# Optimization experiments

Measured on AMD Instinct MI355X. Metric: run time of the kernel, lower is better.

## Reference

```python
import jax, jax.numpy as jnp
import numpy as np

NUM_AUDIOS = 64
NODES_PER = 800
N = NUM_AUDIOS * NODES_PER  # 51200
DEG = 8
E = N * DEG  # 409600
IN_C, HID, OUT, HEADS = 512, 256, 256, 2
NEG_SLOPE = 0.2  # PyG GATConv default


def setup_inputs() -> dict:
    key = jax.random.key(0)
    ks = jax.random.split(key, 12)
    x = jax.random.normal(ks[0], (N, IN_C), jnp.float32)
    # edges strictly inside each audio's node block (PyG batching: no cross-graph edges)
    src_l = jax.random.randint(ks[1], (NUM_AUDIOS, NODES_PER * DEG), 0, NODES_PER)
    dst_l = jax.random.randint(ks[2], (NUM_AUDIOS, NODES_PER * DEG), 0, NODES_PER)
    off = (jnp.arange(NUM_AUDIOS) * NODES_PER)[:, None]
    edge_index = jnp.stack([(src_l + off).reshape(-1), (dst_l + off).reshape(-1)]).astype(jnp.int32)
    batch = jnp.repeat(jnp.arange(NUM_AUDIOS), NODES_PER).astype(jnp.int32)

    def gl(k, shape, fan):
        return (jax.random.normal(k, shape, jnp.float32) / np.sqrt(fan)).astype(jnp.float32)

    W1 = gl(ks[3], (IN_C, HEADS * HID), IN_C)
    a_s1 = gl(ks[4], (HEADS, HID), HID)
    a_d1 = gl(ks[5], (HEADS, HID), HID)
    b1 = jnp.zeros((HID,), jnp.float32)
    W2 = gl(ks[6], (HID, HEADS * OUT), HID)
    a_s2 = gl(ks[7], (HEADS, OUT), OUT)
    a_d2 = gl(ks[8], (HEADS, OUT), OUT)
    b2 = jnp.zeros((OUT,), jnp.float32)
    w_att = gl(ks[9], (OUT, 1), OUT)
    b_att = jnp.zeros((1,), jnp.float32)
    w_cls = gl(ks[10], (OUT, 2), OUT)
    b_cls = jnp.zeros((2,), jnp.float32)
    return dict(x=x, edge_index=edge_index, batch=batch,
                W1=W1, a_s1=a_s1, a_d1=a_d1, b1=b1,
                W2=W2, a_s2=a_s2, a_d2=a_d2, b2=b2,
                w_att=w_att, b_att=b_att, w_cls=w_cls, b_cls=b_cls)


def _gat(x, src, dst, W, a_s, a_d, b):
    """PyG GATConv(heads=H, concat=False): linear -> per-edge LeakyReLU scores ->
    softmax over incoming edges (with self-loops) -> scatter-sum -> head-mean + bias."""
    n = x.shape[0]
    H, C = a_s.shape
    h = (x @ W).reshape(n, H, C)                      # [N,H,C]
    al_s = jnp.einsum('nhc,hc->nh', h, a_s)           # [N,H]
    al_d = jnp.einsum('nhc,hc->nh', h, a_d)
    loop = jnp.arange(n, dtype=src.dtype)             # add self-loops (default)
    s = jnp.concatenate([src, loop])
    d = jnp.concatenate([dst, loop])
    e = jax.nn.leaky_relu(al_s[s] + al_d[d], NEG_SLOPE)  # [E+N,H]
    mx = jax.ops.segment_max(e, d, num_segments=n)
    w = jnp.exp(e - mx[d])
    den = jax.ops.segment_sum(w, d, num_segments=n)
    alpha = w / den[d]
    out = jax.ops.segment_sum(h[s] * alpha[:, :, None], d, num_segments=n)  # [N,H,C]
    return out.mean(axis=1) + b


def reference(x, edge_index, batch, W1, a_s1, a_d1, b1, W2, a_s2, a_d2, b2,
              w_att, b_att, w_cls, b_cls):
    src, dst = edge_index[0], edge_index[1]
    h = jax.nn.relu(_gat(x, src, dst, W1, a_s1, a_d1, b1))
    node_emb = _gat(h, src, dst, W2, a_s2, a_d2, b2)
    # per-audio temporal attention: softmax over nodes within each audio segment.
    # (edges never cross audio boundaries, so the per-subgraph GAT re-run in the
    #  original Python loop equals the full-graph GAT restricted to each segment.)
    logits = node_emb @ w_att + b_att                 # [N,1]
    mx = jax.ops.segment_max(logits, batch, num_segments=NUM_AUDIOS)
    w = jnp.exp(logits - mx[batch])
    den = jax.ops.segment_sum(w, batch, num_segments=NUM_AUDIOS)
    attn = w / den[batch]                             # [N,1]
    attended = jax.ops.segment_sum(attn * node_emb, batch, num_segments=NUM_AUDIOS)  # [A,OUT]
    audio_result = attended @ w_cls + b_cls           # [A,2]
    return node_emb, audio_result
```

## Files before the change

### kernel.cpp

```cpp
#include <hip/hip_runtime.h>
#include <cstdint>
#include <cstddef>

#define NUM_AUDIOS 64
#define NODES_PER  800
#define NN         51200
#define EE         409600

typedef __attribute__((ext_vector_type(8))) unsigned short ushort8;
typedef __attribute__((ext_vector_type(4))) unsigned short ushort4v;
typedef __attribute__((ext_vector_type(8))) __bf16 bf16x8;
typedef __attribute__((ext_vector_type(4))) float f32x4;

__device__ __forceinline__ float b2f(unsigned short h) {
  return __uint_as_float(((unsigned)h) << 16);
}
__device__ __forceinline__ unsigned short f2b(float f) {
  unsigned u = __float_as_uint(f);
  u += 0x7fffu + ((u >> 16) & 1u);
  return (unsigned short)(u >> 16);
}
__device__ __forceinline__ float lrelu(float v) { return v > 0.f ? v : 0.2f * v; }

#define P_AS1 0
#define P_AD1 512
#define P_B1  1024
#define P_AS2 1536
#define P_AD2 2048
#define P_B2  2560
#define P_WATT 3072
#define P_BATT 3328
#define P_WCLS 3336
#define P_BCLS 3848

__global__ __launch_bounds__(256) void detect_k(const unsigned short* __restrict__ x,
                                                int* __restrict__ flag) {
  __shared__ int s;
  if (threadIdx.x == 0) s = 0;
  __syncthreads();
  int big = 0;
  for (int i = threadIdx.x; i < 4096; i += 256) {
    const float v = b2f(x[i]);
    if (!(__builtin_fabsf(v) <= 1e4f)) big = 1;
  }
  if (big) atomicOr(&s, 1);
  __syncthreads();
  if (threadIdx.x == 0) *flag = s;
}

__global__ __launch_bounds__(256) void conv_x_k(const void* __restrict__ xraw,
                                                unsigned short* __restrict__ x16,
                                                const int* __restrict__ flag) {
  const size_t i = ((size_t)blockIdx.x * 256 + threadIdx.x) * 4;
  if (*flag) {
    const float4 v = *(const float4*)((const float*)xraw + i);
    ushort4v o;
    o[0] = f2b(v.x); o[1] = f2b(v.y); o[2] = f2b(v.z); o[3] = f2b(v.w);
    *(ushort4v*)(x16 + i) = o;
  } else {
    *(ushort4v*)(x16 + i) = *(const ushort4v*)((const unsigned short*)xraw + i);
  }
}

__global__ __launch_bounds__(256) void conv_params_k(
    const void* p0, const void* p1, const void* p2, const void* p3, const void* p4,
    const void* p5, const void* p6, const void* p7, const void* p8, const void* p9,
    unsigned short* __restrict__ dst, const int* __restrict__ flag) {
  const void* srcs[10] = {p0, p1, p2, p3, p4, p5, p6, p7, p8, p9};
  const int offs[10] = {P_AS1, P_AD1, P_B1, P_AS2, P_AD2, P_B2, P_WATT, P_BATT, P_WCLS, P_BCLS};
  const int lens[10] = {512, 512, 256, 512, 512, 256, 256, 1, 512, 2};
  const int b = blockIdx.x;
  const int f = *flag;
  for (int i = threadIdx.x; i < lens[b]; i += 256) {
    dst[offs[b] + i] = f ? f2b(((const float*)srcs[b])[i])
                         : ((const unsigned short*)srcs[b])[i];
  }
}

__global__ __launch_bounds__(256) void transpose_k(const void* __restrict__ W,
                                                   unsigned short* __restrict__ WT,
                                                   const int* __restrict__ flag,
                                                   int K, int Nc) {
  const int idx = blockIdx.x * 256 + threadIdx.x;
  const int n = idx / K, k = idx - n * K;
  WT[idx] = (*flag) ? f2b(((const float*)W)[(size_t)k * Nc + n])
                    : ((const unsigned short*)W)[(size_t)k * Nc + n];
}

__global__ __launch_bounds__(256) void gemm_bt(const unsigned short* __restrict__ A,
                                               const unsigned short* __restrict__ BT,
                                               unsigned short* __restrict__ C,
                                               int K, int Nn) {
  __shared__ unsigned short As[128 * 32];
  __shared__ unsigned short Bs[128 * 32];
  const int tid = threadIdx.x;
  const int wave = tid >> 6, lane = tid & 63;
  const int m0 = blockIdx.y * 128, n0 = blockIdx.x * 128;
  const int wm = wave >> 1, wn = wave & 1;
  const int row = lane & 15, quad = lane >> 4;
  f32x4 acc[4][4];
#pragma unroll
  for (int i = 0; i < 4; ++i)
#pragma unroll
    for (int j = 0; j < 4; ++j) acc[i][j] = (f32x4){0.f, 0.f, 0.f, 0.f};

  for (int k0 = 0; k0 < K; k0 += 32) {
#pragma unroll
    for (int r = 0; r < 2; ++r) {
      const int cc = r * 256 + wave * 64 + lane;
      const int arow = cc >> 2, kc = (cc & 3) * 8;
      __builtin_amdgcn_global_load_lds(
          (const __attribute__((address_space(1))) void*)(A + (size_t)(m0 + arow) * K + k0 + kc),
          (__attribute__((address_space(3))) void*)(As + (size_t)(r * 256 + wave * 64) * 8),
          16, 0, 0);
      __builtin_amdgcn_global_load_lds(
          (const __attribute__((address_space(1))) void*)(BT + (size_t)(n0 + arow) * K + k0 + kc),
          (__attribute__((address_space(3))) void*)(Bs + (size_t)(r * 256 + wave * 64) * 8),
          16, 0, 0);
    }
    __syncthreads();

    bf16x8 af[4], bq[4];
#pragma unroll
    for (int i = 0; i < 4; ++i) {
      af[i] = *(const bf16x8*)&As[(wm * 64 + i * 16 + row) * 32 + quad * 8];
      bq[i] = *(const bf16x8*)&Bs[(wn * 64 + i * 16 + row) * 32 + quad * 8];
    }
#pragma unroll
    for (int i = 0; i < 4; ++i)
#pragma unroll
      for (int j = 0; j < 4; ++j)
        acc[i][j] = __builtin_amdgcn_mfma_f32_16x16x32_bf16(af[i], bq[j], acc[i][j], 0, 0, 0);
    __syncthreads();
  }

  const int col = lane & 15;
#pragma unroll
  for (int i = 0; i < 4; ++i)
#pragma unroll
    for (int j = 0; j < 4; ++j)
#pragma unroll
      for (int r = 0; r < 4; ++r) {
        const int gm = m0 + wm * 64 + i * 16 + quad * 4 + r;
        const int gn = n0 + wn * 64 + j * 16 + col;
        C[(size_t)gm * Nn + gn] = f2b(acc[i][j][r]);
      }
}

__global__ __launch_bounds__(256) void al_k(const unsigned short* __restrict__ h,
                                            const unsigned short* __restrict__ a_s,
                                            const unsigned short* __restrict__ a_d,
                                            float* __restrict__ al_s, float* __restrict__ al_d) {
  const int wave = threadIdx.x >> 6, lane = threadIdx.x & 63;
  const int n = blockIdx.x * 4 + wave;
  const ushort8 hv = *(const ushort8*)&h[(size_t)n * 512 + lane * 8];
  const ushort8 sv = *(const ushort8*)&a_s[lane * 8];
  const ushort8 dv = *(const ushort8*)&a_d[lane * 8];
  float ps = 0.f, pd = 0.f;
#pragma unroll
  for (int j = 0; j < 8; ++j) {
    const float hf = b2f(hv[j]);
    ps += hf * b2f(sv[j]);
    pd += hf * b2f(dv[j]);
  }
#pragma unroll
  for (int off = 1; off < 32; off <<= 1) {
    ps += __shfl_xor(ps, off);
    pd += __shfl_xor(pd, off);
  }
  if ((lane & 31) == 0) {
    const int head = lane >> 5;
    al_s[n * 2 + head] = ps;
    al_d[n * 2 + head] = pd;
  }
}

__global__ __launch_bounds__(256) void hist_k(const int* __restrict__ dst, int* __restrict__ counts) {
  const int e = blockIdx.x * 256 + threadIdx.x;
  atomicAdd(&counts[dst[e]], 1);
}

__global__ __launch_bounds__(256) void rowptr_k(const int* __restrict__ counts, int* __restrict__ row_ptr) {
  __shared__ int sh[800];
  __shared__ int pre[200];
  const int a = blockIdx.x, t = threadIdx.x;
  for (int i = t; i < 800; i += 256) sh[i] = counts[a * 800 + i];
  __syncthreads();
  if (t < 200) pre[t] = sh[t * 4] + sh[t * 4 + 1] + sh[t * 4 + 2] + sh[t * 4 + 3];
  __syncthreads();
  if (t == 0) {
    int run = 0;
    for (int i = 0; i < 200; ++i) { const int v = pre[i]; pre[i] = run; run += v; }
  }
  __syncthreads();
  if (t < 200) {
    int b = a * 6400 + pre[t];
#pragma unroll
    for (int j = 0; j < 4; ++j) { row_ptr[a * 800 + t * 4 + j] = b; b += sh[t * 4 + j]; }
  }
}

__global__ __launch_bounds__(256) void scatter_k(const int* __restrict__ src, const int* __restrict__ dst,
                                                 const int* __restrict__ row_ptr, int* __restrict__ cursor,
                                                 int* __restrict__ ssrc) {
  const int e = blockIdx.x * 256 + threadIdx.x;
  const int d = dst[e];
  const int p = atomicAdd(&cursor[d], 1);
  ssrc[row_ptr[d] + p] = src[e];
}

__global__ __launch_bounds__(256) void agg_k(const unsigned short* __restrict__ h,
                                             const float* __restrict__ al_s, const float* __restrict__ al_d,
                                             const int* __restrict__ row_ptr, const int* __restrict__ counts,
                                             const int* __restrict__ ssrc, const unsigned short* __restrict__ bias,
                                             unsigned short* __restrict__ out, int do_relu,
                                             void* __restrict__ out2, const int* __restrict__ flagp,
                                             const unsigned short* __restrict__ watt,
                                             float* __restrict__ lg) {
  const int wave = threadIdx.x >> 6, lane = threadIdx.x & 63;
  const int b = blockIdx.x;
  const int g = b & 7, r = b >> 3;
  const int a = g + 8 * (r / 200);
  const int chunk = r % 200;
  const int n = a * 800 + chunk * 4 + wave;
  const int head = lane >> 5;
  const int hl = lane & 31;
  const int hsel = lane & 32;
  const int deg = counts[n];
  const int base = row_ptr[n];
  const float ald = al_d[n * 2 + head];
  const float self_e = lrelu(al_s[n * 2 + head] + ald);

  float m = -1e30f;
  for (int i = hl; i < deg; i += 32) {
    const int s = ssrc[base + i];
    m = fmaxf(m, al_s[s * 2 + head]);
  }
#pragma unroll
  for (int off = 1; off < 32; off <<= 1) m = fmaxf(m, __shfl_xor(m, off));
  const float mx = fmaxf(lrelu(m + ald), self_e);

  const float w_self = __expf(self_e - mx);
  float acc[8];
  {
    const ushort8 hv = *(const ushort8*)&h[(unsigned)(n * 512 + lane * 8)];
#pragma unroll
    for (int j = 0; j < 8; ++j) acc[j] = w_self * b2f(hv[j]);
  }
  float dpart = 0.f;
  for (int t0 = 0; t0 < deg; t0 += 32) {
    const int cnt = min(32, deg - t0);
    int s = 0; float w = 0.f;
    if (hl < cnt) {
      s = ssrc[base + t0 + hl];
      w = __expf(lrelu(al_s[s * 2 + head] + ald) - mx);
      dpart += w;
    }
    for (int i = 0; i < cnt; ++i) {
      const float wb = __shfl(w, hsel + i);
      const int sb = __shfl(s, hsel + i);
      const ushort8 hv = *(const ushort8*)&h[(unsigned)(sb * 512 + lane * 8)];
#pragma unroll
      for (int j = 0; j < 8; ++j) acc[j] += wb * b2f(hv[j]);
    }
  }
#pragma unroll
  for (int off = 1; off < 32; off <<= 1) dpart += __shfl_xor(dpart, off);
  const float inv = 1.f / (w_self + dpart);

  const int c0 = hl * 8;
  ushort8 res;
  float ov[8];
#pragma unroll
  for (int j = 0; j < 8; ++j) {
    const float mine = acc[j] * inv;
    const float other = __shfl_xor(mine, 32);
    float o = (mine + other) * 0.5f + b2f(bias[c0 + j]);
    if (do_relu) o = fmaxf(o, 0.f);
    ov[j] = o;
    res[j] = f2b(o);
  }
  if (lane < 32) {
    *(ushort8*)&out[(unsigned)(n * 256 + c0)] = res;
    if (out2) {
      if (*flagp) {
        float4* p = (float4*)((float*)out2 + (size_t)n * 256 + c0);
        p[0] = (float4){ov[0], ov[1], ov[2], ov[3]};
        p[1] = (float4){ov[4], ov[5], ov[6], ov[7]};
      } else {
        *(ushort8*)((unsigned short*)out2 + (size_t)n * 256 + c0) = res;
      }
    }
    if (lg) {
      const ushort8 wv = *(const ushort8*)&watt[c0];
      float d = 0.f;
#pragma unroll
      for (int j = 0; j < 8; ++j) d += ov[j] * b2f(wv[j]);
#pragma unroll
      for (int off = 1; off < 32; off <<= 1) d += __shfl_xor(d, off);
      if (hl == 0) lg[n] = d + b2f(watt[256]);
    }
  }
}

__global__ __launch_bounds__(256) void stats_k(const float* __restrict__ lg,
                                               float* __restrict__ mxv, float* __restrict__ invv) {
  __shared__ float red[256];
  const int a = blockIdx.x, t = threadIdx.x;
  float m = -1e30f;
  for (int i = t; i < 800; i += 256) m = fmaxf(m, lg[a * 800 + i]);
  red[t] = m; __syncthreads();
  for (int s = 128; s >= 1; s >>= 1) { if (t < s) red[t] = fmaxf(red[t], red[t + s]); __syncthreads(); }
  const float mx = red[0];
  __syncthreads();
  float sum = 0.f;
  for (int i = t; i < 800; i += 256) sum += __expf(lg[a * 800 + i] - mx);
  red[t] = sum; __syncthreads();
  for (int s = 128; s >= 1; s >>= 1) { if (t < s) red[t] += red[t + s]; __syncthreads(); }
  if (t == 0) { mxv[a] = mx; invv[a] = 1.f / red[0]; }
}

__global__ __launch_bounds__(256) void attended_k(const unsigned short* __restrict__ emb,
                                                  const float* __restrict__ lg,
                                                  const float* __restrict__ mxv,
                                                  const float* __restrict__ invv,
                                                  float* __restrict__ attended) {
  const int b = blockIdx.x;
  const int a = b >> 3, chunk = b & 7;
  const int t = threadIdx.x;
  __shared__ float ws[100];
  const int i0 = chunk * 100;
  const float mx = mxv[a], inv = invv[a];
  if (t < 100) ws[t] = __expf(lg[a * 800 + i0 + t] - mx) * inv;
  __syncthreads();
  float acc = 0.f;
  const unsigned short* base = emb + ((size_t)(a * 800 + i0)) * 256 + t;
#pragma unroll 4
  for (int j = 0; j < 100; ++j) acc += ws[j] * b2f(base[(size_t)j * 256]);
  atomicAdd(&attended[a * 256 + t], acc);
}

__global__ __launch_bounds__(256) void cls_k(const float* __restrict__ attended,
                                             const unsigned short* __restrict__ params,
                                             void* __restrict__ out, const int* __restrict__ flag) {
  __shared__ float red[256];
  const int a = blockIdx.x, t = threadIdx.x;
  const float v = attended[a * 256 + t];
  const float p0 = v * b2f(params[P_WCLS + t * 2]);
  const float p1 = v * b2f(params[P_WCLS + t * 2 + 1]);
  red[t] = p0; __syncthreads();
  for (int s = 128; s >= 1; s >>= 1) { if (t < s) red[t] += red[t + s]; __syncthreads(); }
  const float r0 = red[0];
  __syncthreads();
  red[t] = p1; __syncthreads();
  for (int s = 128; s >= 1; s >>= 1) { if (t < s) red[t] += red[t + s]; __syncthreads(); }
  const float r1 = red[0];
  if (t == 0) {
    const float o0 = r0 + b2f(params[P_BCLS]);
    const float o1 = r1 + b2f(params[P_BCLS + 1]);
    if (*flag) {
      ((float*)out)[(size_t)NN * 256 + a * 2]     = o0;
      ((float*)out)[(size_t)NN * 256 + a * 2 + 1] = o1;
    } else {
      ((unsigned short*)out)[(size_t)NN * 256 + a * 2]     = f2b(o0);
      ((unsigned short*)out)[(size_t)NN * 256 + a * 2 + 1] = f2b(o1);
    }
  }
}

extern "C" void kernel_launch(void* const* d_in, const int* in_sizes, int n_in,
                              void* d_out, int out_size, void* d_ws, size_t ws_size,
                              hipStream_t stream) {
  (void)in_sizes; (void)n_in; (void)out_size; (void)ws_size;
  const void* x_raw  = d_in[0];
  const int*  eidx   = (const int*)d_in[1];
  const int* src = eidx;
  const int* dst = eidx + EE;

  char* ws = (char*)d_ws;
  size_t off = 0;
  auto alloc = [&](size_t bytes) -> void* {
    void* p = ws + off;
    off += (bytes + 255) & ~(size_t)255;
    return p;
  };
  int* flag              = (int*)alloc(256);
  unsigned short* params = (unsigned short*)alloc(4096 * 2);
  unsigned short* W1T    = (unsigned short*)alloc((size_t)512 * 512 * 2);
  unsigned short* W2T    = (unsigned short*)alloc((size_t)512 * 256 * 2);
  unsigned short* x16    = (unsigned short*)alloc((size_t)NN * 512 * 2);
  unsigned short* hbig   = (unsigned short*)alloc((size_t)NN * 512 * 2);
  float* al_s   = (float*)alloc((size_t)NN * 2 * 4);
  float* al_d   = (float*)alloc((size_t)NN * 2 * 4);
  int*   counts = (int*)alloc((size_t)NN * 4);
  int*   rowp   = (int*)alloc((size_t)NN * 4);
  int*   cursor = (int*)alloc((size_t)NN * 4);
  int*   ssrc   = (int*)alloc((size_t)EE * 4);
  float* lg     = (float*)alloc((size_t)NN * 4);
  float* mxv    = (float*)alloc(NUM_AUDIOS * 4);
  float* invv   = (float*)alloc(NUM_AUDIOS * 4);
  float* attended = (float*)alloc((size_t)NUM_AUDIOS * 256 * 4);
  unsigned short* hrel  = x16;
  unsigned short* emb16 = x16 + (size_t)NN * 256;

  detect_k<<<dim3(1), 256, 0, stream>>>((const unsigned short*)x_raw, flag);

  hipMemsetAsync(counts, 0, (size_t)NN * 4, stream);
  hipMemsetAsync(cursor, 0, (size_t)NN * 4, stream);
  hipMemsetAsync(attended, 0, (size_t)NUM_AUDIOS * 256 * 4, stream);

  conv_x_k<<<dim3(NN * 512 / 4 / 256), 256, 0, stream>>>(x_raw, x16, flag);
  conv_params_k<<<dim3(10), 256, 0, stream>>>(d_in[4], d_in[5], d_in[6], d_in[8], d_in[9],
                                              d_in[10], d_in[11], d_in[12], d_in[13], d_in[14],
                                              params, flag);
  transpose_k<<<dim3(512 * 512 / 256), 256, 0, stream>>>(d_in[3], W1T, flag, 512, 512);
  transpose_k<<<dim3(512 * 256 / 256), 256, 0, stream>>>(d_in[7], W2T, flag, 256, 512);

  hist_k<<<dim3(EE / 256), 256, 0, stream>>>(dst, counts);
  rowptr_k<<<dim3(NUM_AUDIOS), 256, 0, stream>>>(counts, rowp);
  scatter_k<<<dim3(EE / 256), 256, 0, stream>>>(src, dst, rowp, cursor, ssrc);

  gemm_bt<<<dim3(4, 400), 256, 0, stream>>>(x16, W1T, hbig, 512, 512);
  al_k<<<dim3(NN / 4), 256, 0, stream>>>(hbig, params + P_AS1, params + P_AD1, al_s, al_d);
  agg_k<<<dim3(NN / 4), 256, 0, stream>>>(hbig, al_s, al_d, rowp, counts, ssrc,
                                          params + P_B1, hrel, 1, nullptr, flag,
                                          params + P_WATT, nullptr);

  gemm_bt<<<dim3(4, 400), 256, 0, stream>>>(hrel, W2T, hbig, 256, 512);
  al_k<<<dim3(NN / 4), 256, 0, stream>>>(hbig, params + P_AS2, params + P_AD2, al_s, al_d);
  agg_k<<<dim3(NN / 4), 256, 0, stream>>>(hbig, al_s, al_d, rowp, counts, ssrc,
                                          params + P_B2, emb16, 0, d_out, flag,
                                          params + P_WATT, lg);

  stats_k<<<dim3(NUM_AUDIOS), 256, 0, stream>>>(lg, mxv, invv);
  attended_k<<<dim3(NUM_AUDIOS * 8), 256, 0, stream>>>(emb16, lg, mxv, invv, attended);
  cls_k<<<dim3(NUM_AUDIOS), 256, 0, stream>>>(attended, params, d_out, flag);
}
```

Baseline: 448.0 us.

## Fuse attention-logit dots into GEMM epilogue and merge prologue kernels

The per-node attention dot products (al_s/al_d) are now computed in the GEMM epilogue from the fp32 accumulators, using shuffle reductions and atomicAdd into zero-initialised buffers. This removes the separate al_k pass that re-read the hidden matrix. The input conversion, parameter conversion, weight transposes and edge histogram are merged into one multi-role kernel, and the three memsets are folded into a zeroing prologue kernel. The changes trade several launches and one large read for extra atomics. Logits now come from unrounded fp32 accumulators rather than bf16 values, so numerics shift slightly.

```diff
diff --git a/kernel.cpp b/kernel.cpp
--- a/kernel.cpp
+++ b/kernel.cpp
@@ -33,64 +33,117 @@
 #define P_WCLS 3336
 #define P_BCLS 3848
 
-__global__ __launch_bounds__(256) void detect_k(const unsigned short* __restrict__ x,
-                                                int* __restrict__ flag) {
-  __shared__ int s;
-  if (threadIdx.x == 0) s = 0;
-  __syncthreads();
-  int big = 0;
-  for (int i = threadIdx.x; i < 4096; i += 256) {
-    const float v = b2f(x[i]);
-    if (!(__builtin_fabsf(v) <= 1e4f)) big = 1;
-  }
-  if (big) atomicOr(&s, 1);
-  __syncthreads();
-  if (threadIdx.x == 0) *flag = s;
-}
-
-__global__ __launch_bounds__(256) void conv_x_k(const void* __restrict__ xraw,
-                                                unsigned short* __restrict__ x16,
-                                                const int* __restrict__ flag) {
-  const size_t i = ((size_t)blockIdx.x * 256 + threadIdx.x) * 4;
-  if (*flag) {
-    const float4 v = *(const float4*)((const float*)xraw + i);
-    ushort4v o;
-    o[0] = f2b(v.x); o[1] = f2b(v.y); o[2] = f2b(v.z); o[3] = f2b(v.w);
-    *(ushort4v*)(x16 + i) = o;
-  } else {
-    *(ushort4v*)(x16 + i) = *(const ushort4v*)((const unsigned short*)xraw + i);
-  }
-}
-
-__global__ __launch_bounds__(256) void conv_params_k(
+#define ZERO_F4 132096
+#define ZERO_BLOCKS 516
+
+__global__ __launch_bounds__(256) void prolog0_k(float4* __restrict__ zbase,
+                                                 const unsigned short* __restrict__ x,
+                                                 int* __restrict__ flag) {
+  const int i = blockIdx.x * 256 + threadIdx.x;
+  if (i < ZERO_F4) zbase[i] = (float4){0.f, 0.f, 0.f, 0.f};
+  if (blockIdx.x == 0) {
+    __shared__ int s;
+    if (threadIdx.x == 0) s = 0;
+    __syncthreads();
+    int big = 0;
+    for (int k = threadIdx.x; k < 4096; k += 256) {
+      const float v = b2f(x[k]);
+      if (!(__builtin_fabsf(v) <= 1e4f)) big = 1;
+    }
+    if (big) atomicOr(&s, 1);
+    __syncthreads();
+    if (threadIdx.x == 0) *flag = s;
+  }
+}
+
+#define PB_CONV 25600
+#define PB_PAR  (PB_CONV + 10)
+#define PB_T1   (PB_PAR + 1024)
+#define PB_T2   (PB_T1 + 512)
+#define PB_HIST (PB_T2 + 1600)
+
+__global__ __launch_bounds__(256) void prep_k(
+    const void* __restrict__ xraw, unsigned short* __restrict__ x16,
+    const void* __restrict__ W1, unsigned short* __restrict__ W1T,
+    const void* __restrict__ W2, unsigned short* __restrict__ W2T,
     const void* p0, const void* p1, const void* p2, const void* p3, const void* p4,
     const void* p5, const void* p6, const void* p7, const void* p8, const void* p9,
-    unsigned short* __restrict__ dst, const int* __restrict__ flag) {
-  const void* srcs[10] = {p0, p1, p2, p3, p4, p5, p6, p7, p8, p9};
-  const int offs[10] = {P_AS1, P_AD1, P_B1, P_AS2, P_AD2, P_B2, P_WATT, P_BATT, P_WCLS, P_BCLS};
-  const int lens[10] = {512, 512, 256, 512, 512, 256, 256, 1, 512, 2};
-  const int b = blockIdx.x;
-  const int f = *flag;
-  for (int i = threadIdx.x; i < lens[b]; i += 256) {
-    dst[offs[b] + i] = f ? f2b(((const float*)srcs[b])[i])
-                         : ((const unsigned short*)srcs[b])[i];
-  }
-}
-
-__global__ __launch_bounds__(256) void transpose_k(const void* __restrict__ W,
-                                                   unsigned short* __restrict__ WT,
-                                                   const int* __restrict__ flag,
-                                                   int K, int Nc) {
-  const int idx = blockIdx.x * 256 + threadIdx.x;
-  const int n = idx / K, k = idx - n * K;
-  WT[idx] = (*flag) ? f2b(((const float*)W)[(size_t)k * Nc + n])
-                    : ((const unsigned short*)W)[(size_t)k * Nc + n];
+    unsigned short* __restrict__ params,
+    const int* __restrict__ dst, int* __restrict__ counts,
+    const int* __restrict__ flagp) {
+  const int b = blockIdx.x, tid = threadIdx.x;
+  const int f = *flagp;
+  if (b < PB_CONV) {
+    const size_t i = ((size_t)b * 256 + tid) * 4;
+    if (f) {
+      const float4 v = *(const float4*)((const float*)xraw + i);
+      ushort4v o;
+      o[0] = f2b(v.x); o[1] = f2b(v.y); o[2] = f2b(v.z); o[3] = f2b(v.w);
+      *(ushort4v*)(x16 + i) = o;
+    } else {
+      *(ushort4v*)(x16 + i) = *(const ushort4v*)((const unsigned short*)xraw + i);
+    }
+  } else if (b < PB_PAR) {
+    const void* srcs[10] = {p0, p1, p2, p3, p4, p5, p6, p7, p8, p9};
+    const int offs[10] = {P_AS1, P_AD1, P_B1, P_AS2, P_AD2, P_B2, P_WATT, P_BATT, P_WCLS, P_BCLS};
+    const int lens[10] = {512, 512, 256, 512, 512, 256, 256, 1, 512, 2};
+    const int s = b - PB_CONV;
+    for (int i = tid; i < lens[s]; i += 256)
+      params[offs[s] + i] = f ? f2b(((const float*)srcs[s])[i])
+                              : ((const unsigned short*)srcs[s])[i];
+  } else if (b < PB_T1) {
+    const int idx = (b - PB_PAR) * 256 + tid;
+    const int n = idx >> 9, k = idx & 511;
+    W1T[idx] = f ? f2b(((const float*)W1)[(size_t)k * 512 + n])
+                 : ((const unsigned short*)W1)[(size_t)k * 512 + n];
+  } else if (b < PB_T2) {
+    const int idx = (b - PB_T1) * 256 + tid;
+    const int n = idx >> 8, k = idx & 255;
+    W2T[idx] = f ? f2b(((const float*)W2)[(size_t)k * 512 + n])
+                 : ((const unsigned short*)W2)[(size_t)k * 512 + n];
+  } else {
+    const int e = (b - PB_T2) * 256 + tid;
+    atomicAdd(&counts[dst[e]], 1);
+  }
+}
+
+__global__ __launch_bounds__(256) void rowptr_k(const int* __restrict__ counts, int* __restrict__ row_ptr) {
+  __shared__ int sh[800];
+  __shared__ int pre[200];
+  const int a = blockIdx.x, t = threadIdx.x;
+  for (int i = t; i < 800; i += 256) sh[i] = counts[a * 800 + i];
+  __syncthreads();
+  if (t < 200) pre[t] = sh[t * 4] + sh[t * 4 + 1] + sh[t * 4 + 2] + sh[t * 4 + 3];
+  __syncthreads();
+  if (t == 0) {
+    int run = 0;
+    for (int i = 0; i < 200; ++i) { const int v = pre[i]; pre[i] = run; run += v; }
+  }
+  __syncthreads();
+  if (t < 200) {
+    int b = a * 6400 + pre[t];
+#pragma unroll
+    for (int j = 0; j < 4; ++j) { row_ptr[a * 800 + t * 4 + j] = b; b += sh[t * 4 + j]; }
+  }
+}
+
+__global__ __launch_bounds__(256) void scatter_k(const int* __restrict__ src, const int* __restrict__ dst,
+                                                 const int* __restrict__ row_ptr, int* __restrict__ cursor,
+                                                 int* __restrict__ ssrc) {
+  const int e = blockIdx.x * 256 + threadIdx.x;
+  const int d = dst[e];
+  const int p = atomicAdd(&cursor[d], 1);
+  ssrc[row_ptr[d] + p] = src[e];
 }
 
 __global__ __launch_bounds__(256) void gemm_bt(const unsigned short* __restrict__ A,
                                                const unsigned short* __restrict__ BT,
                                                unsigned short* __restrict__ C,
-                                               int K, int Nn) {
+                                               int K, int Nn,
+                                               const unsigned short* __restrict__ a_s,
+                                               const unsigned short* __restrict__ a_d,
+                                               float* __restrict__ al_s,
+                                               float* __restrict__ al_d) {
   __shared__ unsigned short As[128 * 32];
   __shared__ unsigned short Bs[128 * 32];
   const int tid = threadIdx.x;
@@ -145,68 +198,35 @@
         const int gn = n0 + wn * 64 + j * 16 + col;
         C[(size_t)gm * Nn + gn] = f2b(acc[i][j][r]);
       }
-}
-
-__global__ __launch_bounds__(256) void al_k(const unsigned short* __restrict__ h,
-                                            const unsigned short* __restrict__ a_s,
-                                            const unsigned short* __restrict__ a_d,
-                                            float* __restrict__ al_s, float* __restrict__ al_d) {
-  const int wave = threadIdx.x >> 6, lane = threadIdx.x & 63;
-  const int n = blockIdx.x * 4 + wave;
-  const ushort8 hv = *(const ushort8*)&h[(size_t)n * 512 + lane * 8];
-  const ushort8 sv = *(const ushort8*)&a_s[lane * 8];
-  const ushort8 dv = *(const ushort8*)&a_d[lane * 8];
-  float ps = 0.f, pd = 0.f;
-#pragma unroll
-  for (int j = 0; j < 8; ++j) {
-    const float hf = b2f(hv[j]);
-    ps += hf * b2f(sv[j]);
-    pd += hf * b2f(dv[j]);
-  }
-#pragma unroll
-  for (int off = 1; off < 32; off <<= 1) {
-    ps += __shfl_xor(ps, off);
-    pd += __shfl_xor(pd, off);
-  }
-  if ((lane & 31) == 0) {
-    const int head = lane >> 5;
-    al_s[n * 2 + head] = ps;
-    al_d[n * 2 + head] = pd;
-  }
-}
-
-__global__ __launch_bounds__(256) void hist_k(const int* __restrict__ dst, int* __restrict__ counts) {
-  const int e = blockIdx.x * 256 + threadIdx.x;
-  atomicAdd(&counts[dst[e]], 1);
-}
-
-__global__ __launch_bounds__(256) void rowptr_k(const int* __restrict__ counts, int* __restrict__ row_ptr) {
-  __shared__ int sh[800];
-  __shared__ int pre[200];
-  const int a = blockIdx.x, t = threadIdx.x;
-  for (int i = t; i < 800; i += 256) sh[i] = counts[a * 800 + i];
-  __syncthreads();
-  if (t < 200) pre[t] = sh[t * 4] + sh[t * 4 + 1] + sh[t * 4 + 2] + sh[t * 4 + 3];
-  __syncthreads();
-  if (t == 0) {
-    int run = 0;
-    for (int i = 0; i < 200; ++i) { const int v = pre[i]; pre[i] = run; run += v; }
-  }
-  __syncthreads();
-  if (t < 200) {
-    int b = a * 6400 + pre[t];
-#pragma unroll
-    for (int j = 0; j < 4; ++j) { row_ptr[a * 800 + t * 4 + j] = b; b += sh[t * 4 + j]; }
-  }
-}
-
-__global__ __launch_bounds__(256) void scatter_k(const int* __restrict__ src, const int* __restrict__ dst,
-                                                 const int* __restrict__ row_ptr, int* __restrict__ cursor,
-                                                 int* __restrict__ ssrc) {
-  const int e = blockIdx.x * 256 + threadIdx.x;
-  const int d = dst[e];
-  const int p = atomicAdd(&cursor[d], 1);
-  ssrc[row_ptr[d] + p] = src[e];
+
+  {
+    const int head = (n0 + wn * 64) >> 8;
+    float as4[4], ad4[4];
+#pragma unroll
+    for (int j = 0; j < 4; ++j) {
+      const int gn = n0 + wn * 64 + j * 16 + col;
+      as4[j] = b2f(a_s[gn]);
+      ad4[j] = b2f(a_d[gn]);
+    }
+#pragma unroll
+    for (int i = 0; i < 4; ++i)
+#pragma unroll
+      for (int r = 0; r < 4; ++r) {
+        float ps = 0.f, pd = 0.f;
+#pragma unroll
+        for (int j = 0; j < 4; ++j) { ps += acc[i][j][r] * as4[j]; pd += acc[i][j][r] * ad4[j]; }
+#pragma unroll
+        for (int off = 1; off < 16; off <<= 1) {
+          ps += __shfl_xor(ps, off);
+          pd += __shfl_xor(pd, off);
+        }
+        if (col == 0) {
+          const int gm = m0 + wm * 64 + i * 16 + quad * 4 + r;
+          atomicAdd(&al_s[gm * 2 + head], ps);
+          atomicAdd(&al_d[gm * 2 + head], pd);
+        }
+      }
+  }
 }
 
 __global__ __launch_bounds__(256) void agg_k(const unsigned short* __restrict__ h,
@@ -390,45 +410,42 @@
   unsigned short* W2T    = (unsigned short*)alloc((size_t)512 * 256 * 2);
   unsigned short* x16    = (unsigned short*)alloc((size_t)NN * 512 * 2);
   unsigned short* hbig   = (unsigned short*)alloc((size_t)NN * 512 * 2);
-  float* al_s   = (float*)alloc((size_t)NN * 2 * 4);
-  float* al_d   = (float*)alloc((size_t)NN * 2 * 4);
-  int*   counts = (int*)alloc((size_t)NN * 4);
+  int*   counts   = (int*)alloc((size_t)NN * 4);
+  int*   cursor   = (int*)alloc((size_t)NN * 4);
+  float* attended = (float*)alloc((size_t)NUM_AUDIOS * 256 * 4);
+  float* al_s1    = (float*)alloc((size_t)NN * 2 * 4);
+  float* al_d1    = (float*)alloc((size_t)NN * 2 * 4);
+  float* al_s2    = (float*)alloc((size_t)NN * 2 * 4);
+  float* al_d2    = (float*)alloc((size_t)NN * 2 * 4);
   int*   rowp   = (int*)alloc((size_t)NN * 4);
-  int*   cursor = (int*)alloc((size_t)NN * 4);
   int*   ssrc   = (int*)alloc((size_t)EE * 4);
   float* lg     = (float*)alloc((size_t)NN * 4);
   float* mxv    = (float*)alloc(NUM_AUDIOS * 4);
   float* invv   = (float*)alloc(NUM_AUDIOS * 4);
-  float* attended = (float*)alloc((size_t)NUM_AUDIOS * 256 * 4);
   unsigned short* hrel  = x16;
   unsigned short* emb16 = x16 + (size_t)NN * 256;
 
-  detect_k<<<dim3(1), 256, 0, stream>>>((const unsigned short*)x_raw, flag);
-
-  hipMemsetAsync(counts, 0, (size_t)NN * 4, stream);
-  hipMemsetAsync(cursor, 0, (size_t)NN * 4, stream);
-  hipMemsetAsync(attended, 0, (size_t)NUM_AUDIOS * 256 * 4, stream);
-
-  conv_x_k<<<dim3(NN * 512 / 4 / 256), 256, 0, stream>>>(x_raw, x16, flag);
-  conv_params_k<<<dim3(10), 256, 0, stream>>>(d_in[4], d_in[5], d_in[6], d_in[8], d_in[9],
-                                              d_in[10], d_in[11], d_in[12], d_in[13], d_in[14],
-                                              params, flag);
-  transpose_k<<<dim3(512 * 512 / 256), 256, 0, stream>>>(d_in[3], W1T, flag, 512, 512);
-  transpose_k<<<dim3(512 * 256 / 256), 256, 0, stream>>>(d_in[7], W2T, flag, 256, 512);
-
-  hist_k<<<dim3(EE / 256), 256, 0, stream>>>(dst, counts);
+  prolog0_k<<<dim3(ZERO_BLOCKS), 256, 0, stream>>>((float4*)counts,
+                                                   (const unsigned short*)x_raw, flag);
+
+  prep_k<<<dim3(PB_HIST), 256, 0, stream>>>(
+      x_raw, x16, d_in[3], W1T, d_in[7], W2T,
+      d_in[4], d_in[5], d_in[6], d_in[8], d_in[9],
+      d_in[10], d_in[11], d_in[12], d_in[13], d_in[14],
+      params, dst, counts, flag);
+
   rowptr_k<<<dim3(NUM_AUDIOS), 256, 0, stream>>>(counts, rowp);
   scatter_k<<<dim3(EE / 256), 256, 0, stream>>>(src, dst, rowp, cursor, ssrc);
 
-  gemm_bt<<<dim3(4, 400), 256, 0, stream>>>(x16, W1T, hbig, 512, 512);
-  al_k<<<dim3(NN / 4), 256, 0, stream>>>(hbig, params + P_AS1, params + P_AD1, al_s, al_d);
-  agg_k<<<dim3(NN / 4), 256, 0, stream>>>(hbig, al_s, al_d, rowp, counts, ssrc,
+  gemm_bt<<<dim3(4, 400), 256, 0, stream>>>(x16, W1T, hbig, 512, 512,
+                                            params + P_AS1, params + P_AD1, al_s1, al_d1);
+  agg_k<<<dim3(NN / 4), 256, 0, stream>>>(hbig, al_s1, al_d1, rowp, counts, ssrc,
                                           params + P_B1, hrel, 1, nullptr, flag,
                                           params + P_WATT, nullptr);
 
-  gemm_bt<<<dim3(4, 400), 256, 0, stream>>>(hrel, W2T, hbig, 256, 512);
-  al_k<<<dim3(NN / 4), 256, 0, stream>>>(hbig, params + P_AS2, params + P_AD2, al_s, al_d);
-  agg_k<<<dim3(NN / 4), 256, 0, stream>>>(hbig, al_s, al_d, rowp, counts, ssrc,
+  gemm_bt<<<dim3(4, 400), 256, 0, stream>>>(hrel, W2T, hbig, 256, 512,
+                                            params + P_AS2, params + P_AD2, al_s2, al_d2);
+  agg_k<<<dim3(NN / 4), 256, 0, stream>>>(hbig, al_s2, al_d2, rowp, counts, ssrc,
                                           params + P_B2, emb16, 0, d_out, flag,
                                           params + P_WATT, lg);
 
```

After: 440.4 us. Within noise of the previous version (-1.7%).
